# Kernel optimization log

Measured on AMD Instinct MI355X. Metric: run time of the kernel, lower is better.

## Reference

```python
import jax, jax.numpy as jnp
import numpy as np

VAR_NUM = 96
EMBED_TIME = 128
INPUT_DIM = VAR_NUM * 2 + EMBED_TIME  # 320
ATTN_DIM = 64
N_HEADS = 8
ALL_DIM = ATTN_DIM * N_HEADS  # 512
B, N = 8, 2048
NEG_INF = -1e9  # finite stand-in for masked_fill(-inf); safe under softmax


def setup_inputs() -> dict:
    key = jax.random.key(0)
    ks = jax.random.split(key, 16)
    s = lambda d: 1.0 / np.sqrt(d)
    return {
        "times_in": jax.random.uniform(ks[0], (B, N), jnp.float32),
        "data_in": jax.random.normal(ks[1], (B, N, VAR_NUM), jnp.float32),
        "mask_in": jnp.ones((B, N, VAR_NUM), jnp.float32),
        "exist_times": jax.random.randint(ks[2], (B, N), 0, 2, jnp.int32),
        # TimeEmbedding params
        "w_per": jax.random.normal(ks[3], (1, EMBED_TIME - 1), jnp.float32),
        "b_per": jnp.zeros((EMBED_TIME - 1,), jnp.float32),
        "w_lin": jax.random.normal(ks[4], (1, 1), jnp.float32),
        "b_lin": jnp.zeros((1,), jnp.float32),
        # Attention params
        "Wq": jax.random.normal(ks[5], (INPUT_DIM, ALL_DIM), jnp.float32) * s(INPUT_DIM),
        "bq": jnp.zeros((ALL_DIM,), jnp.float32),
        "Wk": jax.random.normal(ks[6], (INPUT_DIM, ALL_DIM), jnp.float32) * s(INPUT_DIM),
        "bk": jnp.zeros((ALL_DIM,), jnp.float32),
        "Wv": jax.random.normal(ks[7], (INPUT_DIM, ALL_DIM), jnp.float32) * s(INPUT_DIM),
        "bv": jnp.zeros((ALL_DIM,), jnp.float32),
        "Wfc": jax.random.normal(ks[8], (ALL_DIM, ATTN_DIM), jnp.float32) * s(ALL_DIM),
        "bfc": jnp.zeros((ATTN_DIM,), jnp.float32),
    }


def reference(times_in, data_in, mask_in, exist_times,
              w_per, b_per, w_lin, b_lin,
              Wq, bq, Wk, bk, Wv, bv, Wfc, bfc):
    b, n = times_in.shape
    tt = times_in[..., None]  # [b, n, 1]
    # TimeEmbedding: [linear(tt), sin(periodic(tt))]
    te = jnp.concatenate([tt @ w_lin + b_lin, jnp.sin(tt @ w_per + b_per)], axis=-1)
    x = jnp.concatenate([data_in, mask_in, te], axis=-1)  # [b, n, INPUT_DIM]

    def heads(w, bias):
        return (x @ w + bias).reshape(b, n, N_HEADS, ATTN_DIM).transpose(0, 2, 1, 3)

    q, k, v = heads(Wq, bq), heads(Wk, bk), heads(Wv, bv)  # [b, h, n, d]
    # NOTE: custom scale uses sqrt(input_dim), not sqrt(head_dim)
    scores = jnp.einsum("bhqd,bhkd->bhqk", q, k) / jnp.sqrt(jnp.float32(INPUT_DIM))
    m = (exist_times != 0)
    scores = jnp.where(m[:, None, None, :], scores, NEG_INF)  # mask keys
    attn = jax.nn.softmax(scores, axis=-1)  # dropout p=0 in eval reference
    out = jnp.einsum("bhqk,bhkd->bhqd", attn, v)
    out = jnp.where(m[:, None, :, None], out, 0.0)  # zero masked query rows
    out = out.transpose(0, 2, 1, 3).reshape(b, n, ALL_DIM)
    return out @ Wfc + bfc  # [b, n, ATTN_DIM]
```

## Files before the change

kernel.cpp:

```cpp
#include <hip/hip_runtime.h>

#define N_ 2048
#define BN 16384
#define IN_DIM 320
#define QKV_N 1536
#define ALPHA 0.08064911f

typedef float f32x4 __attribute__((ext_vector_type(4)));
typedef short v8s __attribute__((ext_vector_type(8)));
typedef unsigned int u32x2 __attribute__((ext_vector_type(2)));

__device__ __forceinline__ short f2b(float f) {
  unsigned u = __builtin_bit_cast(unsigned, f);
  u = u + 0x7fff + ((u >> 16) & 1);
  return (short)(u >> 16);
}

__device__ __forceinline__ void gload16(const short* g, void* l) {
  __builtin_amdgcn_global_load_lds((const __attribute__((address_space(1))) void*)g,
                                   (__attribute__((address_space(3))) void*)l, 16, 0, 0);
}

__device__ __forceinline__ int piperm(int t) {
  return ((t >> 5) & 1) * 32 + ((t >> 2) & 3) * 8 + ((t >> 4) & 1) * 4 + (t & 3);
}

__global__ void build_x(const float* __restrict__ times, const float* __restrict__ data,
                        const float* __restrict__ maskv, const float* __restrict__ w_per,
                        const float* __restrict__ b_per, const float* __restrict__ w_lin,
                        const float* __restrict__ b_lin, short* __restrict__ x) {
  int row = blockIdx.x;
  int t = threadIdx.x;
  float tt = times[row];
  short* xr = x + (size_t)row * IN_DIM;
  const float* dr = data + (size_t)row * 96;
  const float* mr = maskv + (size_t)row * 96;
  if (t < 96) { xr[t] = f2b(dr[t]); xr[96 + t] = f2b(mr[t]); }
  float val;
  if (t == 0) val = tt * w_lin[0] + b_lin[0];
  else        val = __sinf(tt * w_per[t - 1] + b_per[t - 1]);
  xr[192 + t] = f2b(val);
}

__global__ void scan_mask(const int* __restrict__ exist, int* __restrict__ prefix,
                          int* __restrict__ ntg, int* __restrict__ totals,
                          short* __restrict__ flagsc) {
  __shared__ int sums[256];
  int b = blockIdx.x;
  int t = threadIdx.x;
  const int* e = exist + b * 2048;
  int loc[8];
  int s = 0;
#pragma unroll
  for (int j = 0; j < 8; ++j) { loc[j] = s; s += (e[t * 8 + j] != 0) ? 1 : 0; }
  sums[t] = s;
  __syncthreads();
  for (int d = 1; d < 256; d <<= 1) {
    int v = (t >= d) ? sums[t - d] : 0;
    __syncthreads();
    sums[t] += v;
    __syncthreads();
  }
  int total = sums[255];
  int base = (t == 0) ? 0 : sums[t - 1];
#pragma unroll
  for (int j = 0; j < 8; ++j) prefix[b * 2048 + t * 8 + j] = base + loc[j];
  if (t == 0) { ntg[b] = (total + 63) >> 6; totals[b] = total; }
#pragma unroll
  for (int j = 0; j < 8; ++j) {
    int slot = t * 8 + j;
    flagsc[b * 2048 + (slot & ~63) + piperm(slot & 63)] =
        (slot < total) ? (short)0x3F80 : (short)0;
  }
}

__global__ void transpose_w(const float* __restrict__ Wq, const float* __restrict__ Wk,
                            const float* __restrict__ Wv, const float* __restrict__ Wfc,
                            short* __restrict__ Wt, short* __restrict__ WfcT) {
  int idx = blockIdx.x * 256 + threadIdx.x;
  if (idx < QKV_N * IN_DIM) {
    int n = idx / IN_DIM, kk = idx - n * IN_DIM;
    const float* W = (n < 512) ? Wq : (n < 1024 ? Wk : Wv);
    Wt[idx] = f2b(W[(size_t)kk * 512 + (n & 511)]);
  } else {
    int j = idx - QKV_N * IN_DIM;
    int d = j >> 9, kk = j & 511;
    WfcT[j] = f2b(Wfc[kk * 64 + d]);
  }
}

__launch_bounds__(256)
__global__ void qkv_gemm(const short* __restrict__ x, const short* __restrict__ Wt,
                         const float* __restrict__ bq, const float* __restrict__ bk,
                         const float* __restrict__ bv, const int* __restrict__ exist,
                         const int* __restrict__ prefix,
                         short* __restrict__ q, short* __restrict__ kc, short* __restrict__ vc) {
  __shared__ short As[128][32];
  __shared__ short Bs[128][32];
  int bm = blockIdx.x;
  int bn = blockIdx.y;
  int tid = threadIdx.x, wave = tid >> 6, lane = tid & 63;
  int wm = wave >> 1, wn = wave & 1;
  int l16 = lane & 15, lh = lane >> 4;
  int srow[2], sgc[2];
#pragma unroll
  for (int s = 0; s < 2; ++s) {
    srow[s] = (wave + 4 * s) * 16 + (lane >> 2);
    sgc[s] = (lane & 3) ^ (srow[s] & 3);
  }
  const short* xa = x + (size_t)(bm * 128) * IN_DIM;
  const short* wa = Wt + (size_t)(bn * 128) * IN_DIM;
  int rpos = (lh ^ (l16 & 3)) * 8;
  f32x4 acc[4][4] = {};
  for (int kt = 0; kt < 10; ++kt) {
    int k0 = kt * 32;
#pragma unroll
    for (int s = 0; s < 2; ++s) {
      gload16(xa + (size_t)srow[s] * IN_DIM + k0 + sgc[s] * 8,
              (char*)&As[0][0] + (wave + 4 * s) * 1024);
      gload16(wa + (size_t)srow[s] * IN_DIM + k0 + sgc[s] * 8,
              (char*)&Bs[0][0] + (wave + 4 * s) * 1024);
    }
    __syncthreads();
    v8s af[4], bfr[4];
#pragma unroll
    for (int m = 0; m < 4; ++m) af[m] = *(const v8s*)&As[wm * 64 + m * 16 + l16][rpos];
#pragma unroll
    for (int n = 0; n < 4; ++n) bfr[n] = *(const v8s*)&Bs[wn * 64 + n * 16 + l16][rpos];
#pragma unroll
    for (int m = 0; m < 4; ++m)
#pragma unroll
      for (int n = 0; n < 4; ++n)
        acc[m][n] = __builtin_amdgcn_mfma_f32_16x16x32_bf16(af[m], bfr[n], acc[m][n], 0, 0, 0);
    __syncthreads();
  }
  int w = bn >> 2;
  if (w == 0) {
#pragma unroll
    for (int m = 0; m < 4; ++m) {
      int row0 = bm * 128 + wm * 64 + m * 16 + lh * 4;
#pragma unroll
      for (int n = 0; n < 4; ++n) {
        int c = (bn * 128 + wn * 64 + n * 16 + l16) & 511;
        float bb = bq[c];
        int h = c >> 6, d = c & 63;
#pragma unroll
        for (int r = 0; r < 4; ++r) {
          int rr = row0 + r;
          int b = rr >> 11, ntok = rr & 2047;
          q[(((size_t)(b * 8 + h) * N_ + ntok) << 6) + d] = f2b((acc[m][n][r] + bb) * ALPHA);
        }
      }
    }
  } else {
    short* dbuf = (w == 1) ? kc : vc;
    const float* bias = (w == 1) ? bk : bv;
#pragma unroll
    for (int m = 0; m < 4; ++m) {
      int row0 = bm * 128 + wm * 64 + m * 16 + lh * 4;
      int exr[4], dstr[4];
#pragma unroll
      for (int r = 0; r < 4; ++r) { exr[r] = exist[row0 + r]; dstr[r] = prefix[row0 + r]; }
      int b = row0 >> 11;
#pragma unroll
      for (int n = 0; n < 4; ++n) {
        int c = (bn * 128 + wn * 64 + n * 16 + l16) & 511;
        float bb = bias[c];
        int h = c >> 6, d = c & 63;
#pragma unroll
        for (int r = 0; r < 4; ++r)
          if (exr[r])
            dbuf[(((size_t)(b * 8 + h) * N_ + dstr[r]) << 6) + d] = f2b(acc[m][n][r] + bb);
      }
    }
  }
}

__launch_bounds__(256)
__global__ void fragmentize(short* __restrict__ kc, short* __restrict__ vc,
                            const int* __restrict__ ntg, const int* __restrict__ totals) {
  __shared__ short Ks[64][66];
  __shared__ short Vs[64][66];
  int bh = blockIdx.x;
  int b = bh >> 3;
  int nt = ntg[b], total = totals[b];
  int tid = threadIdx.x;
  size_t hb = (size_t)bh * N_ * 64;
  for (int tile = blockIdx.y; tile < nt; tile += 8) {
    int base = tile * 64;
#pragma unroll
    for (int s = 0; s < 2; ++s) {
      int c = tid + s * 256, r = c >> 3, c8 = c & 7;
      v8s kv = {0, 0, 0, 0, 0, 0, 0, 0};
      v8s vv = {0, 0, 0, 0, 0, 0, 0, 0};
      if (base + r < total) {
        kv = *(const v8s*)&kc[hb + (size_t)(base + r) * 64 + c8 * 8];
        vv = *(const v8s*)&vc[hb + (size_t)(base + r) * 64 + c8 * 8];
      }
      *(v8s*)&Ks[r][c8 * 8] = kv;
      *(v8s*)&Vs[r][c8 * 8] = vv;
    }
    __syncthreads();
#pragma unroll
    for (int s = 0; s < 2; ++s) {
      int c = tid + s * 256;
      int i = c >> 6, lh2 = (c >> 4) & 3, r16 = c & 15;
      *(v8s*)&kc[hb + (size_t)tile * 4096 + c * 8] =
          *(const v8s*)&Ks[(i >> 1) * 16 + r16][(i & 1) * 32 + lh2 * 8];
      int l16 = c & 15, lh = (c >> 4) & 3, kc2 = (c >> 6) & 1, n2 = c >> 7;
      int d = n2 * 16 + l16;
      v8s o;
#pragma unroll
      for (int jj = 0; jj < 8; ++jj) {
        int t2 = kc2 * 32 + (jj >> 2) * 16 + lh * 4 + (jj & 3);
        o[jj] = Vs[t2][d];
      }
      *(v8s*)&vc[hb + (size_t)tile * 4096 + c * 8] = o;
    }
    __syncthreads();
  }
}

__launch_bounds__(256, 2)
__global__ void attn_kernel(const short* __restrict__ q, const short* __restrict__ kT,
                            const short* __restrict__ vT, const short* __restrict__ flagsc,
                            const int* __restrict__ ntg, const int* __restrict__ exist,
                            short* __restrict__ att) {
  int bx = blockIdx.x;
  int bh = ((bx >> 6) << 3) | (bx & 7);
  int qblk = (bx >> 3) & 7;
  int b = bh >> 3, h = bh & 7;
  int tid = threadIdx.x, wave = tid >> 6, lane = tid & 63;
  int l16 = lane & 15, lh = lane >> 4;
  int q0 = qblk * 256 + wave * 64;
  int nt = ntg[b];
  const short* qp = q + (size_t)bh * N_ * 64;
  const short* kpt = kT + (size_t)bh * 131072;
  const short* vpt = vT + (size_t)bh * 131072;
  const short* fpt = flagsc + b * N_;
  const int* ex = exist + b * N_;
  v8s qf[4][2];
#pragma unroll
  for (int m = 0; m < 4; ++m)
#pragma unroll
    for (int kcx = 0; kcx < 2; ++kcx)
      qf[m][kcx] = *(const v8s*)&qp[(size_t)(q0 + m * 16 + l16) * 64 + kcx * 32 + lh * 8];
  f32x4 oacc[4][4] = {};
  f32x4 lacc[4] = {};
  const f32x4 zf = {0.f, 0.f, 0.f, 0.f};
  int voff = lane * 8;
  v8s kf[8], vf[8], ff[2];
#pragma unroll
  for (int i = 0; i < 8; ++i) {
    kf[i] = *(const v8s*)&kpt[i * 512 + voff];
    vf[i] = *(const v8s*)&vpt[i * 512 + voff];
  }
  ff[0] = *(const v8s*)&fpt[lh * 8];
  ff[1] = *(const v8s*)&fpt[32 + lh * 8];
#pragma unroll 1
  for (int kt = 0; kt < nt; ++kt) {
    const short* kn = kpt + (size_t)(kt + 1) * 4096;
    const short* vn = vpt + (size_t)(kt + 1) * 4096;
    const short* fn = fpt + (kt + 1) * 64;
    bool pre = (kt + 1 < nt);
#pragma unroll
    for (int mh = 0; mh < 2; ++mh) {
      f32x4 sacc[2][4];
#pragma unroll
      for (int n = 0; n < 4; ++n)
#pragma unroll
        for (int mm = 0; mm < 2; ++mm) {
          sacc[mm][n] = __builtin_amdgcn_mfma_f32_16x16x32_bf16(kf[n * 2], qf[mh * 2 + mm][0], zf, 0, 0, 0);
          sacc[mm][n] = __builtin_amdgcn_mfma_f32_16x16x32_bf16(kf[n * 2 + 1], qf[mh * 2 + mm][1], sacc[mm][n], 0, 0, 0);
        }
      if (mh == 1 && pre)
#pragma unroll
        for (int i = 0; i < 8; ++i) kf[i] = *(const v8s*)&kn[i * 512 + voff];
      v8s pf[2][2];
#pragma unroll
      for (int mm = 0; mm < 2; ++mm)
#pragma unroll
        for (int kcx = 0; kcx < 2; ++kcx)
#pragma unroll
          for (int half = 0; half < 2; ++half) {
            int n = kcx * 2 + half;
            float p0 = __builtin_amdgcn_exp2f(sacc[mm][n][0]);
            float p1 = __builtin_amdgcn_exp2f(sacc[mm][n][1]);
            float p2 = __builtin_amdgcn_exp2f(sacc[mm][n][2]);
            float p3 = __builtin_amdgcn_exp2f(sacc[mm][n][3]);
            uint w0, w1;
            asm("v_cvt_pk_bf16_f32 %0, %1, %2" : "=v"(w0) : "v"(p0), "v"(p1));
            asm("v_cvt_pk_bf16_f32 %0, %1, %2" : "=v"(w1) : "v"(p2), "v"(p3));
            ((uint*)&pf[mm][kcx])[half * 2]     = w0;
            ((uint*)&pf[mm][kcx])[half * 2 + 1] = w1;
          }
#pragma unroll
      for (int kcx = 0; kcx < 2; ++kcx) {
#pragma unroll
        for (int mm = 0; mm < 2; ++mm)
          lacc[mh * 2 + mm] = __builtin_amdgcn_mfma_f32_16x16x32_bf16(pf[mm][kcx], ff[kcx], lacc[mh * 2 + mm], 0, 0, 0);
#pragma unroll
        for (int n = 0; n < 4; ++n)
#pragma unroll
          for (int mm = 0; mm < 2; ++mm)
            oacc[mh * 2 + mm][n] = __builtin_amdgcn_mfma_f32_16x16x32_bf16(pf[mm][kcx], vf[n * 2 + kcx], oacc[mh * 2 + mm][n], 0, 0, 0);
      }
    }
    if (pre) {
#pragma unroll
      for (int i = 0; i < 8; ++i) vf[i] = *(const v8s*)&vn[i * 512 + voff];
      ff[0] = *(const v8s*)&fn[lh * 8];
      ff[1] = *(const v8s*)&fn[32 + lh * 8];
    }
  }
#pragma unroll
  for (int m = 0; m < 4; ++m)
#pragma unroll
    for (int r = 0; r < 4; ++r) {
      int row = q0 + m * 16 + lh * 4 + r;
      float qm = (ex[row] != 0) ? 1.f : 0.f;
      float inv = qm / fmaxf(lacc[m][r], 1e-20f);
#pragma unroll
      for (int n = 0; n < 4; ++n)
        att[((size_t)(b * N_ + row)) * 512 + h * 64 + n * 16 + l16] = f2b(oacc[m][n][r] * inv);
    }
}

__launch_bounds__(256)
__global__ void out_gemm(const short* __restrict__ att, const short* __restrict__ WfcT,
                         const float* __restrict__ bfc, float* __restrict__ out) {
  __shared__ short As[128][40];
  __shared__ short Bs[64][40];
  int bm = blockIdx.x;
  int tid = threadIdx.x, wave = tid >> 6, lane = tid & 63;
  int l16 = lane & 15, lh = lane >> 4;
  f32x4 acc[2][4] = {};
  for (int kt = 0; kt < 16; ++kt) {
    int k0 = kt * 32;
#pragma unroll
    for (int s = 0; s < 2; ++s) {
      int c = tid + s * 256;
      int r = c >> 2, c8 = c & 3;
      *(v8s*)&As[r][c8 * 8] = *(const v8s*)&att[(size_t)(bm * 128 + r) * 512 + k0 + c8 * 8];
    }
    { int r = tid >> 2, c8 = tid & 3;
      if (r < 64) *(v8s*)&Bs[r][c8 * 8] = *(const v8s*)&WfcT[(size_t)r * 512 + k0 + c8 * 8]; }
    __syncthreads();
    v8s bfr[4];
#pragma unroll
    for (int n = 0; n < 4; ++n) bfr[n] = *(const v8s*)&Bs[n * 16 + l16][lh * 8];
#pragma unroll
    for (int m = 0; m < 2; ++m) {
      v8s af = *(const v8s*)&As[wave * 32 + m * 16 + l16][lh * 8];
#pragma unroll
      for (int n = 0; n < 4; ++n)
        acc[m][n] = __builtin_amdgcn_mfma_f32_16x16x32_bf16(af, bfr[n], acc[m][n], 0, 0, 0);
    }
    __syncthreads();
  }
#pragma unroll
  for (int m = 0; m < 2; ++m)
#pragma unroll
    for (int n = 0; n < 4; ++n) {
      float bb = bfc[n * 16 + l16];
#pragma unroll
      for (int r = 0; r < 4; ++r) {
        int row = bm * 128 + wave * 32 + m * 16 + lh * 4 + r;
        out[(size_t)row * 64 + n * 16 + l16] = acc[m][n][r] + bb;
      }
    }
}

extern "C" void kernel_launch(void* const* d_in, const int* in_sizes, int n_in,
                              void* d_out, int out_size, void* d_ws, size_t ws_size,
                              hipStream_t stream) {
  const float* times = (const float*)d_in[0];
  const float* data  = (const float*)d_in[1];
  const float* maskv = (const float*)d_in[2];
  const int*   exist = (const int*)d_in[3];
  const float* w_per = (const float*)d_in[4];
  const float* b_per = (const float*)d_in[5];
  const float* w_lin = (const float*)d_in[6];
  const float* b_lin = (const float*)d_in[7];
  const float* Wq  = (const float*)d_in[8];
  const float* bq  = (const float*)d_in[9];
  const float* Wk  = (const float*)d_in[10];
  const float* bk  = (const float*)d_in[11];
  const float* Wv  = (const float*)d_in[12];
  const float* bv  = (const float*)d_in[13];
  const float* Wfc = (const float*)d_in[14];
  const float* bfc = (const float*)d_in[15];
  float* out = (float*)d_out;

  char* ws = (char*)d_ws;
  short* x     = (short*)(ws);
  short* Wt    = (short*)(ws + 10485760);
  short* WfcT  = (short*)(ws + 11468800);
  short* qb    = (short*)(ws + 11534336);
  short* kcb   = (short*)(ws + 28311552);
  short* vcb   = (short*)(ws + 45088768);
  short* att   = (short*)(ws + 61865984);
  short* flagsc= (short*)(ws + 78643200);
  int*   prefix= (int*)(ws + 78675968);
  int*   ntg   = (int*)(ws + 78741504);
  int*   totals= (int*)(ws + 78741536);

  build_x<<<BN, 128, 0, stream>>>(times, data, maskv, w_per, b_per, w_lin, b_lin, x);
  scan_mask<<<8, 256, 0, stream>>>(exist, prefix, ntg, totals, flagsc);
  transpose_w<<<2048, 256, 0, stream>>>(Wq, Wk, Wv, Wfc, Wt, WfcT);
  qkv_gemm<<<dim3(128, 12), 256, 0, stream>>>(x, Wt, bq, bk, bv, exist, prefix, qb, kcb, vcb);
  fragmentize<<<dim3(64, 8), 256, 0, stream>>>(kcb, vcb, ntg, totals);
  attn_kernel<<<512, 256, 0, stream>>>(qb, kcb, vcb, flagsc, ntg, exist, att);
  out_gemm<<<128, 256, 0, stream>>>(att, WfcT, bfc, out);
}
```

Baseline: 108.5 us.

## Double-buffer QKV GEMM LDS tiles and halve attention query rows per wave

The QKV GEMM now keeps two LDS buffers and issues the global-to-LDS load for the next K slice before computing the current one. This overlaps load latency with MFMA work and drops one barrier per iteration. The attention kernel now gives each wave 32 query rows instead of 64 and launches 1024 blocks instead of 512, giving more waves to spread across CUs and fewer live registers per wave. The cost is that each K/V tile is re-read from global or cache by twice as many waves, and the MFMA work per fragment load is lower.

```diff
diff --git a/kernel.cpp b/kernel.cpp
--- a/kernel.cpp
+++ b/kernel.cpp
@@ -95,8 +95,8 @@
                          const float* __restrict__ bv, const int* __restrict__ exist,
                          const int* __restrict__ prefix,
                          short* __restrict__ q, short* __restrict__ kc, short* __restrict__ vc) {
-  __shared__ short As[128][32];
-  __shared__ short Bs[128][32];
+  __shared__ short As[2][128][32];
+  __shared__ short Bs[2][128][32];
   int bm = blockIdx.x;
   int bn = blockIdx.y;
   int tid = threadIdx.x, wave = tid >> 6, lane = tid & 63;
@@ -111,22 +111,26 @@
   const short* xa = x + (size_t)(bm * 128) * IN_DIM;
   const short* wa = Wt + (size_t)(bn * 128) * IN_DIM;
   int rpos = (lh ^ (l16 & 3)) * 8;
-  f32x4 acc[4][4] = {};
-  for (int kt = 0; kt < 10; ++kt) {
-    int k0 = kt * 32;
+  auto stage = [&](int buf, int k0) {
 #pragma unroll
     for (int s = 0; s < 2; ++s) {
       gload16(xa + (size_t)srow[s] * IN_DIM + k0 + sgc[s] * 8,
-              (char*)&As[0][0] + (wave + 4 * s) * 1024);
+              (char*)&As[buf][0][0] + (wave + 4 * s) * 1024);
       gload16(wa + (size_t)srow[s] * IN_DIM + k0 + sgc[s] * 8,
-              (char*)&Bs[0][0] + (wave + 4 * s) * 1024);
-    }
-    __syncthreads();
+              (char*)&Bs[buf][0][0] + (wave + 4 * s) * 1024);
+    }
+  };
+  f32x4 acc[4][4] = {};
+  stage(0, 0);
+  __syncthreads();
+  for (int kt = 0; kt < 10; ++kt) {
+    int cur = kt & 1;
+    if (kt < 9) stage(cur ^ 1, (kt + 1) * 32);
     v8s af[4], bfr[4];
 #pragma unroll
-    for (int m = 0; m < 4; ++m) af[m] = *(const v8s*)&As[wm * 64 + m * 16 + l16][rpos];
-#pragma unroll
-    for (int n = 0; n < 4; ++n) bfr[n] = *(const v8s*)&Bs[wn * 64 + n * 16 + l16][rpos];
+    for (int m = 0; m < 4; ++m) af[m] = *(const v8s*)&As[cur][wm * 64 + m * 16 + l16][rpos];
+#pragma unroll
+    for (int n = 0; n < 4; ++n) bfr[n] = *(const v8s*)&Bs[cur][wn * 64 + n * 16 + l16][rpos];
 #pragma unroll
     for (int m = 0; m < 4; ++m)
 #pragma unroll
@@ -227,26 +231,26 @@
                             const int* __restrict__ ntg, const int* __restrict__ exist,
                             short* __restrict__ att) {
   int bx = blockIdx.x;
-  int bh = ((bx >> 6) << 3) | (bx & 7);
-  int qblk = (bx >> 3) & 7;
+  int bh = ((bx >> 7) << 3) | (bx & 7);
+  int qblk = (bx >> 3) & 15;
   int b = bh >> 3, h = bh & 7;
   int tid = threadIdx.x, wave = tid >> 6, lane = tid & 63;
   int l16 = lane & 15, lh = lane >> 4;
-  int q0 = qblk * 256 + wave * 64;
+  int q0 = qblk * 128 + wave * 32;
   int nt = ntg[b];
   const short* qp = q + (size_t)bh * N_ * 64;
   const short* kpt = kT + (size_t)bh * 131072;
   const short* vpt = vT + (size_t)bh * 131072;
   const short* fpt = flagsc + b * N_;
   const int* ex = exist + b * N_;
-  v8s qf[4][2];
-#pragma unroll
-  for (int m = 0; m < 4; ++m)
+  v8s qf[2][2];
+#pragma unroll
+  for (int m = 0; m < 2; ++m)
 #pragma unroll
     for (int kcx = 0; kcx < 2; ++kcx)
       qf[m][kcx] = *(const v8s*)&qp[(size_t)(q0 + m * 16 + l16) * 64 + kcx * 32 + lh * 8];
-  f32x4 oacc[4][4] = {};
-  f32x4 lacc[4] = {};
+  f32x4 oacc[2][4] = {};
+  f32x4 lacc[2] = {};
   const f32x4 zf = {0.f, 0.f, 0.f, 0.f};
   int voff = lane * 8;
   v8s kf[8], vf[8], ff[2];
@@ -263,48 +267,45 @@
     const short* vn = vpt + (size_t)(kt + 1) * 4096;
     const short* fn = fpt + (kt + 1) * 64;
     bool pre = (kt + 1 < nt);
-#pragma unroll
-    for (int mh = 0; mh < 2; ++mh) {
-      f32x4 sacc[2][4];
+    f32x4 sacc[2][4];
+#pragma unroll
+    for (int n = 0; n < 4; ++n)
+#pragma unroll
+      for (int mm = 0; mm < 2; ++mm) {
+        sacc[mm][n] = __builtin_amdgcn_mfma_f32_16x16x32_bf16(kf[n * 2], qf[mm][0], zf, 0, 0, 0);
+        sacc[mm][n] = __builtin_amdgcn_mfma_f32_16x16x32_bf16(kf[n * 2 + 1], qf[mm][1], sacc[mm][n], 0, 0, 0);
+      }
+    if (pre)
+#pragma unroll
+      for (int i = 0; i < 8; ++i) kf[i] = *(const v8s*)&kn[i * 512 + voff];
+    v8s pf[2][2];
+#pragma unroll
+    for (int mm = 0; mm < 2; ++mm)
+#pragma unroll
+      for (int kcx = 0; kcx < 2; ++kcx)
+#pragma unroll
+        for (int half = 0; half < 2; ++half) {
+          int n = kcx * 2 + half;
+          float p0 = __builtin_amdgcn_exp2f(sacc[mm][n][0]);
+          float p1 = __builtin_amdgcn_exp2f(sacc[mm][n][1]);
+          float p2 = __builtin_amdgcn_exp2f(sacc[mm][n][2]);
+          float p3 = __builtin_amdgcn_exp2f(sacc[mm][n][3]);
+          uint w0, w1;
+          asm("v_cvt_pk_bf16_f32 %0, %1, %2" : "=v"(w0) : "v"(p0), "v"(p1));
+          asm("v_cvt_pk_bf16_f32 %0, %1, %2" : "=v"(w1) : "v"(p2), "v"(p3));
+          ((uint*)&pf[mm][kcx])[half * 2]     = w0;
+          ((uint*)&pf[mm][kcx])[half * 2 + 1] = w1;
+        }
+#pragma unroll
+    for (int kcx = 0; kcx < 2; ++kcx) {
+#pragma unroll
+      for (int mm = 0; mm < 2; ++mm)
+        lacc[mm] = __builtin_amdgcn_mfma_f32_16x16x32_bf16(pf[mm][kcx], ff[kcx], lacc[mm], 0, 0, 0);
 #pragma unroll
       for (int n = 0; n < 4; ++n)
 #pragma unroll
-        for (int mm = 0; mm < 2; ++mm) {
-          sacc[mm][n] = __builtin_amdgcn_mfma_f32_16x16x32_bf16(kf[n * 2], qf[mh * 2 + mm][0], zf, 0, 0, 0);
-          sacc[mm][n] = __builtin_amdgcn_mfma_f32_16x16x32_bf16(kf[n * 2 + 1], qf[mh * 2 + mm][1], sacc[mm][n], 0, 0, 0);
-        }
-      if (mh == 1 && pre)
-#pragma unroll
-        for (int i = 0; i < 8; ++i) kf[i] = *(const v8s*)&kn[i * 512 + voff];
-      v8s pf[2][2];
-#pragma unroll
-      for (int mm = 0; mm < 2; ++mm)
-#pragma unroll
-        for (int kcx = 0; kcx < 2; ++kcx)
-#pragma unroll
-          for (int half = 0; half < 2; ++half) {
-            int n = kcx * 2 + half;
-            float p0 = __builtin_amdgcn_exp2f(sacc[mm][n][0]);
-            float p1 = __builtin_amdgcn_exp2f(sacc[mm][n][1]);
-            float p2 = __builtin_amdgcn_exp2f(sacc[mm][n][2]);
-            float p3 = __builtin_amdgcn_exp2f(sacc[mm][n][3]);
-            uint w0, w1;
-            asm("v_cvt_pk_bf16_f32 %0, %1, %2" : "=v"(w0) : "v"(p0), "v"(p1));
-            asm("v_cvt_pk_bf16_f32 %0, %1, %2" : "=v"(w1) : "v"(p2), "v"(p3));
-            ((uint*)&pf[mm][kcx])[half * 2]     = w0;
-            ((uint*)&pf[mm][kcx])[half * 2 + 1] = w1;
-          }
-#pragma unroll
-      for (int kcx = 0; kcx < 2; ++kcx) {
-#pragma unroll
         for (int mm = 0; mm < 2; ++mm)
-          lacc[mh * 2 + mm] = __builtin_amdgcn_mfma_f32_16x16x32_bf16(pf[mm][kcx], ff[kcx], lacc[mh * 2 + mm], 0, 0, 0);
-#pragma unroll
-        for (int n = 0; n < 4; ++n)
-#pragma unroll
-          for (int mm = 0; mm < 2; ++mm)
-            oacc[mh * 2 + mm][n] = __builtin_amdgcn_mfma_f32_16x16x32_bf16(pf[mm][kcx], vf[n * 2 + kcx], oacc[mh * 2 + mm][n], 0, 0, 0);
-      }
+          oacc[mm][n] = __builtin_amdgcn_mfma_f32_16x16x32_bf16(pf[mm][kcx], vf[n * 2 + kcx], oacc[mm][n], 0, 0, 0);
     }
     if (pre) {
 #pragma unroll
@@ -314,7 +315,7 @@
     }
   }
 #pragma unroll
-  for (int m = 0; m < 4; ++m)
+  for (int m = 0; m < 2; ++m)
 #pragma unroll
     for (int r = 0; r < 4; ++r) {
       int row = q0 + m * 16 + lh * 4 + r;
@@ -410,6 +411,6 @@
   transpose_w<<<2048, 256, 0, stream>>>(Wq, Wk, Wv, Wfc, Wt, WfcT);
   qkv_gemm<<<dim3(128, 12), 256, 0, stream>>>(x, Wt, bq, bk, bv, exist, prefix, qb, kcb, vcb);
   fragmentize<<<dim3(64, 8), 256, 0, stream>>>(kcb, vcb, ntg, totals);
-  attn_kernel<<<512, 256, 0, stream>>>(qb, kcb, vcb, flagsc, ntg, exist, att);
+  attn_kernel<<<1024, 256, 0, stream>>>(qb, kcb, vcb, flagsc, ntg, exist, att);
   out_gemm<<<128, 256, 0, stream>>>(att, WfcT, bfc, out);
 }
```

After: 119.7 us. +10.4%, slower.
